# Kernel optimization log

Hardware: AMD Instinct MI355X
Metric: run time of the kernel (lower is better)

The kernel has to match this reference:

```python
import jax, jax.numpy as jnp
import numpy as np

NEG = -1000000.0  # mask value used by the torch module


def setup_inputs() -> dict:
    key = jax.random.key(0)
    k1, k2, k3, k4 = jax.random.split(key, 4)
    B, Q, K, D = 16, 2048, 2048, 128
    queries = jax.random.normal(k1, (B, Q, D), dtype=jnp.float32)
    keys = jax.random.normal(k2, (B, K, D), dtype=jnp.float32)
    values = jax.random.normal(k3, (B, K, D), dtype=jnp.float32)
    valid_lens = jax.random.randint(k4, (B,), 0, K, dtype=jnp.int32)
    return {"queries": queries, "keys": keys, "values": values, "valid_lens": valid_lens}


def reference(queries, keys, values, valid_lens):
    d = queries.shape[-1]
    # scores: [B, Q, K]
    scores = jnp.einsum("bqd,bkd->bqk", queries, keys) / jnp.sqrt(jnp.float32(d))
    # mask key positions >= valid_len[b] with the same -1e6 value as torch
    kv_pos = jnp.arange(scores.shape[-1])  # [K]
    mask = kv_pos[None, None, :] < valid_lens[:, None, None]  # [B,1,K]
    scores = jnp.where(mask, scores, NEG)
    attn = jax.nn.softmax(scores, axis=-1)
    # dropout p=0.0 -> identity (module in eval)
    return jnp.einsum("bqk,bkd->bqd", attn, values)
```

## Files before the change

### kernel.cpp

```cpp
#include <hip/hip_runtime.h>
#include <hip/hip_bf16.h>

#define NB    16
#define NQ    2048
#define NKV   2048
#define DH    128
#define KVT   32
#define NT    64
#define TIMG  8192

typedef __attribute__((ext_vector_type(8)))  short  short8;
typedef __attribute__((ext_vector_type(4)))  float  f32x4;
typedef __attribute__((ext_vector_type(2)))  float  f32x2;
typedef __attribute__((ext_vector_type(16))) float  f32x16;
typedef __attribute__((ext_vector_type(2)))  unsigned int u32x2;

__device__ __forceinline__ unsigned short f2bf(float f) {
    union { float f; unsigned int u; } x; x.f = f;
    unsigned int r = (x.u + 0x7fffu + ((x.u >> 16) & 1u)) >> 16;
    return (unsigned short)r;
}

__device__ __forceinline__ float u2f(unsigned int u) {
    union { unsigned int u; float f; } x; x.u = u; return x.f;
}

__device__ __forceinline__ void load_lds16(const void* g, void* l) {
    __builtin_amdgcn_global_load_lds(
        (const __attribute__((address_space(1))) unsigned int*)g,
        (__attribute__((address_space(3))) unsigned int*)l, 16, 0, 0);
}

__global__ __launch_bounds__(256)
void preconv(const float* __restrict__ kg, const float* __restrict__ vg,
             const int* __restrict__ vlg, char* __restrict__ kws,
             char* __restrict__ vws) {
    const int tid = threadIdx.x;
    const int bid = blockIdx.x;
    const int b = bid & 15, t = bid >> 4;
    const int vl = vlg[b];
    const int nt = (vl == 0) ? NT : ((vl + KVT - 1) >> 5);
    if (t >= nt) return;

    const float* kb = kg + ((size_t)b * NKV + t * KVT) * DH;
    const float* vb = vg + ((size_t)b * NKV + t * KVT) * DH;
    char* kimg = kws + (size_t)(b * NT + t) * TIMG;
    char* vimg = vws + (size_t)(b * NT + t) * TIMG;

    #pragma unroll
    for (int p = 0; p < 2; ++p) {
        int idx = p * 256 + tid;
        int kv = idx >> 4, ch = idx & 15;
        f32x4 a = *(const f32x4*)(kb + kv * DH + ch * 8);
        f32x4 c = *(const f32x4*)(kb + kv * DH + ch * 8 + 4);
        union { short8 v; unsigned short u[8]; } w;
        #pragma unroll
        for (int j = 0; j < 4; ++j) { w.u[j] = f2bf(a[j]); w.u[4 + j] = f2bf(c[j]); }
        *(short8*)(kimg + kv * 256 + ((ch * 16) ^ ((kv & 15) << 4))) = w.v;
    }
    #pragma unroll
    for (int p = 0; p < 2; ++p) {
        int task = p * 256 + tid;
        int w = task & 3, d = task >> 2;
        union { short8 v; unsigned short u[8]; } o;
        #pragma unroll
        for (int j = 0; j < 8; ++j) o.u[j] = f2bf(vb[(w * 8 + j) * DH + d]);
        int byte = (d >> 2) * 256 + 16 * ((w + 4 * (d & 3)) ^ ((d >> 2) & 15));
        *(short8*)(vimg + byte) = o.v;
    }
}

__global__ __launch_bounds__(256, 3)
void attn32(const float* __restrict__ qg, const char* __restrict__ kws,
            const char* __restrict__ vws, const int* __restrict__ vlg,
            float* __restrict__ og, unsigned int* __restrict__ opart,
            float* __restrict__ ellg, int S) {
    __shared__ __align__(16) char smem[32768];

    const int tid  = threadIdx.x;
    const int lane = tid & 63;
    const int wv   = tid >> 6;
    const int l31  = lane & 31;
    const int h    = lane >> 5;

    const int bid = blockIdx.x;
    const int b  = bid & 15;
    const int qt = (bid >> 4) & 15;
    const int s  = bid >> 8;
    const int q0 = qt * 128 + wv * 32;
    const int vl = vlg[b];
    const int nt = (vl == 0) ? NT : ((vl + KVT - 1) >> 5);

    if (s >= nt) return;

    const float QS = 1.4426950408889634f * 0.08838834764831845f;
    short8 qw[8];
    {
        const float* qp = qg + ((size_t)b * NQ + q0 + l31) * DH + h * 8;
        #pragma unroll
        for (int c = 0; c < 8; ++c) {
            f32x4 a  = *(const f32x4*)(qp + c * 16);
            f32x4 bb = *(const f32x4*)(qp + c * 16 + 4);
            union { short8 v; unsigned short u[8]; } t;
            #pragma unroll
            for (int j = 0; j < 4; ++j) { t.u[j] = f2bf(a[j] * QS); t.u[4 + j] = f2bf(bb[j] * QS); }
            qw[c] = t.v;
        }
    }

    const float MASKV = (vl == 0) ? 0.0f : -1442695.0f;
    f32x16 oacc[4];
    #pragma unroll
    for (int d = 0; d < 4; ++d) oacc[d] = (f32x16)(0.0f);
    float esum = 0.f;

    const char* kbase = kws + (size_t)b * NT * TIMG;
    const char* vbase = vws + (size_t)b * NT * TIMG;

    auto issue = [&](int t, int pb) {
        const char* ks = kbase + (size_t)t * TIMG;
        const char* vs = vbase + (size_t)t * TIMG;
        char* kd = smem + pb * 8192;
        char* vd = smem + 16384 + pb * 8192;
        #pragma unroll
        for (int i = 0; i < 2; ++i) {
            int off = wv * 2048 + i * 1024;
            load_lds16(ks + off + lane * 16, kd + off);
        }
        #pragma unroll
        for (int i = 0; i < 2; ++i) {
            int off = wv * 2048 + i * 1024;
            load_lds16(vs + off + lane * 16, vd + off);
        }
    };

    issue(s, 0);
    int p = 0;
    const int l15s = (l31 & 15) << 4;

    for (int tt = s; tt < nt; tt += S) {
        asm volatile("s_waitcnt vmcnt(0)" ::: "memory");
        __syncthreads();
        int tn = tt + S;
        if (tn < nt) issue(tn, p ^ 1);

        const char* kb = smem + p * 8192;
        const char* vb = smem + 16384 + p * 8192;

        f32x16 sc = (f32x16)(0.0f);
        __builtin_amdgcn_s_setprio(1);
        #pragma unroll
        for (int c = 0; c < 8; ++c) {
            short8 kf = *(const short8*)(kb + l31 * 256 + ((c * 32 + h * 16) ^ l15s));
            sc = __builtin_amdgcn_mfma_f32_32x32x16_bf16(kf, qw[c], sc, 0, 0, 0);
        }
        __builtin_amdgcn_s_setprio(0);

        if (vl == 0 || tt == nt - 1) {
            int kvb = tt * 32 + 4 * h;
            #pragma unroll
            for (int r = 0; r < 16; ++r) {
                int kvg = kvb + (r & 3) + 8 * (r >> 2);
                if (kvg >= vl) sc[r] = MASKV;
            }
        }

        float pe[16];
        #pragma unroll
        for (int r = 0; r < 16; ++r) pe[r] = __builtin_amdgcn_exp2f(sc[r]);
        esum += (((pe[0] + pe[1]) + (pe[2] + pe[3])) + ((pe[4] + pe[5]) + (pe[6] + pe[7])))
              + (((pe[8] + pe[9]) + (pe[10] + pe[11])) + ((pe[12] + pe[13]) + (pe[14] + pe[15])));

        unsigned int A, B, C, D, E, F, G, H;
        asm("v_cvt_pk_bf16_f32 %0, %1, %2" : "=v"(A) : "v"(pe[0]),  "v"(pe[1]));
        asm("v_cvt_pk_bf16_f32 %0, %1, %2" : "=v"(B) : "v"(pe[2]),  "v"(pe[3]));
        asm("v_cvt_pk_bf16_f32 %0, %1, %2" : "=v"(C) : "v"(pe[4]),  "v"(pe[5]));
        asm("v_cvt_pk_bf16_f32 %0, %1, %2" : "=v"(D) : "v"(pe[6]),  "v"(pe[7]));
        asm("v_cvt_pk_bf16_f32 %0, %1, %2" : "=v"(E) : "v"(pe[8]),  "v"(pe[9]));
        asm("v_cvt_pk_bf16_f32 %0, %1, %2" : "=v"(F) : "v"(pe[10]), "v"(pe[11]));
        asm("v_cvt_pk_bf16_f32 %0, %1, %2" : "=v"(G) : "v"(pe[12]), "v"(pe[13]));
        asm("v_cvt_pk_bf16_f32 %0, %1, %2" : "=v"(H) : "v"(pe[14]), "v"(pe[15]));
        asm("v_permlane32_swap_b32 %0, %1" : "+v"(A), "+v"(C));
        asm("v_permlane32_swap_b32 %0, %1" : "+v"(B), "+v"(D));
        asm("v_permlane32_swap_b32 %0, %1" : "+v"(E), "+v"(G));
        asm("v_permlane32_swap_b32 %0, %1" : "+v"(F), "+v"(H));
        union { short8 v; unsigned int w[4]; } P0, P1;
        P0.w[0] = A; P0.w[1] = B; P0.w[2] = C; P0.w[3] = D;
        P1.w[0] = E; P1.w[1] = F; P1.w[2] = G; P1.w[3] = H;
        short8 pa[2] = { P0.v, P1.v };

        __builtin_amdgcn_s_setprio(1);
        #pragma unroll
        for (int dblk = 0; dblk < 4; ++dblk) {
            int quad = dblk * 8 + (l31 >> 2);
            int xk = quad & 15;
            #pragma unroll
            for (int c16 = 0; c16 < 2; ++c16) {
                int w = c16 * 2 + h;
                short8 vf = *(const short8*)(vb + quad * 256 +
                                             16 * ((w + 4 * (l31 & 3)) ^ xk));
                oacc[dblk] = __builtin_amdgcn_mfma_f32_32x32x16_bf16(vf, pa[c16], oacc[dblk], 0, 0, 0);
            }
        }
        __builtin_amdgcn_s_setprio(0);
        p ^= 1;
    }

    float ea = esum, eb;
    asm volatile("v_mov_b32 %0, %1" : "=v"(eb) : "v"(esum));
    asm("v_permlane32_swap_b32 %0, %1" : "+v"(ea), "+v"(eb));
    float ell = ea + eb;

    __syncthreads();

    if (S > 1 && lane < 32)
        ellg[(size_t)s * NB * NQ + (size_t)b * NQ + q0 + lane] = ell;

    float* tw = (float*)smem + wv * 1120;
    if (lane < 32) tw[1088 + l31] = 1.0f / ell;
    unsigned int* opw = opart + ((size_t)s * NB * NQ + (size_t)b * NQ + q0) * 64;
    float* ogp = og + ((size_t)b * NQ + q0) * DH;

    #pragma unroll
    for (int dblk = 0; dblk < 4; ++dblk) {
        #pragma unroll
        for (int r = 0; r < 16; ++r) {
            int dd = (r & 3) + 8 * (r >> 2) + 4 * h;
            tw[l31 * 34 + dd] = oacc[dblk][r];
        }
        #pragma unroll
        for (int pp = 0; pp < 8; ++pp) {
            int qq = pp * 4 + (lane >> 4);
            int cc = lane & 15;
            f32x2 v = *(f32x2*)(tw + qq * 34 + cc * 2);
            if (S == 1) {
                float rl = tw[1088 + qq];
                f32x2 o = { v[0] * rl, v[1] * rl };
                *(f32x2*)(ogp + (size_t)qq * DH + dblk * 32 + cc * 2) = o;
            } else {
                unsigned int w;
                asm("v_cvt_pk_bf16_f32 %0, %1, %2" : "=v"(w) : "v"(v[0]), "v"(v[1]));
                opw[(size_t)qq * 64 + dblk * 16 + cc] = w;
            }
        }
    }
}

__global__ __launch_bounds__(256)
void combine(const unsigned int* __restrict__ opart, const float* __restrict__ ellg,
             const int* __restrict__ vlg, float* __restrict__ og, int S) {
    int idx = blockIdx.x * 256 + threadIdx.x;
    int row = idx >> 5;
    int c   = idx & 31;
    int b   = row >> 11;
    int vl  = vlg[b];
    int nact = (vl == 0) ? NT : ((vl + KVT - 1) >> 5);
    if (nact > S) nact = S;
    float a0 = 0.f, a1 = 0.f, a2 = 0.f, a3 = 0.f, l = 0.f;
    for (int s = 0; s < nact; ++s) {
        l += ellg[(size_t)s * NB * NQ + row];
        u32x2 w = *(const u32x2*)(opart + ((size_t)s * NB * NQ + row) * 64 + c * 2);
        a0 += u2f(w[0] << 16); a1 += u2f(w[0] & 0xffff0000u);
        a2 += u2f(w[1] << 16); a3 += u2f(w[1] & 0xffff0000u);
    }
    float rl = 1.0f / l;
    f32x4 o = { a0 * rl, a1 * rl, a2 * rl, a3 * rl };
    *(f32x4*)(og + (size_t)row * DH + c * 4) = o;
}

extern "C" void kernel_launch(void* const* d_in, const int* in_sizes, int n_in,
                              void* d_out, int out_size, void* d_ws, size_t ws_size,
                              hipStream_t stream) {
    const float* q  = (const float*)d_in[0];
    const float* k  = (const float*)d_in[1];
    const float* v  = (const float*)d_in[2];
    const int*   vl = (const int*)d_in[3];
    float* o = (float*)d_out;

    const size_t IMG     = (size_t)NB * NT * TIMG;
    const size_t ELL_OFF = 2 * IMG;
    const size_t ELL_MAX = (size_t)8 * NB * NQ * 4;
    const size_t OP_OFF  = ELL_OFF + ELL_MAX;
    const size_t OP_ONE  = (size_t)NB * NQ * DH * 2;

    int S = 1;
    if      (ws_size >= OP_OFF + 8 * OP_ONE) S = 8;
    else if (ws_size >= OP_OFF + 4 * OP_ONE) S = 4;
    else if (ws_size >= OP_OFF + 2 * OP_ONE) S = 2;

    char* kws = (char*)d_ws;
    char* vws = (char*)d_ws + IMG;
    float* ellg = (float*)((char*)d_ws + ELL_OFF);
    unsigned int* opart = (unsigned int*)((char*)d_ws + OP_OFF);

    preconv<<<dim3(NB * NT), dim3(256), 0, stream>>>(k, v, vl, kws, vws);
    attn32<<<dim3(256 * S), dim3(256), 0, stream>>>(q, kws, vws, vl, o, opart, ellg, S);
    if (S > 1)
        combine<<<dim3(NB * NQ * 32 / 256), dim3(256), 0, stream>>>(opart, ellg, vl, o, S);
}
```

Measured before the change: 70.19 us.

## Load K/V MFMA fragments directly from global in lane-order layout, drop LDS staging

```diff
diff --git a/kernel.cpp b/kernel.cpp
--- a/kernel.cpp
+++ b/kernel.cpp
@@ -23,12 +23,6 @@
 
 __device__ __forceinline__ float u2f(unsigned int u) {
     union { unsigned int u; float f; } x; x.u = u; return x.f;
-}
-
-__device__ __forceinline__ void load_lds16(const void* g, void* l) {
-    __builtin_amdgcn_global_load_lds(
-        (const __attribute__((address_space(1))) unsigned int*)g,
-        (__attribute__((address_space(3))) unsigned int*)l, 16, 0, 0);
 }
 
 __global__ __launch_bounds__(256)
@@ -47,49 +41,51 @@
     char* kimg = kws + (size_t)(b * NT + t) * TIMG;
     char* vimg = vws + (size_t)(b * NT + t) * TIMG;
 
+    const int lane = tid & 63;
+    const int l31  = lane & 31;
+    const int h    = (lane >> 5) & 1;
+
     #pragma unroll
     for (int p = 0; p < 2; ++p) {
-        int idx = p * 256 + tid;
-        int kv = idx >> 4, ch = idx & 15;
-        f32x4 a = *(const f32x4*)(kb + kv * DH + ch * 8);
-        f32x4 c = *(const f32x4*)(kb + kv * DH + ch * 8 + 4);
+        int c = (tid >> 6) + p * 4;
+        int d0 = c * 16 + h * 8;
+        f32x4 a  = *(const f32x4*)(kb + l31 * DH + d0);
+        f32x4 b2 = *(const f32x4*)(kb + l31 * DH + d0 + 4);
         union { short8 v; unsigned short u[8]; } w;
         #pragma unroll
-        for (int j = 0; j < 4; ++j) { w.u[j] = f2bf(a[j]); w.u[4 + j] = f2bf(c[j]); }
-        *(short8*)(kimg + kv * 256 + ((ch * 16) ^ ((kv & 15) << 4))) = w.v;
+        for (int j = 0; j < 4; ++j) { w.u[j] = f2bf(a[j]); w.u[4 + j] = f2bf(b2[j]); }
+        *(short8*)(kimg + c * 1024 + lane * 16) = w.v;
     }
     #pragma unroll
     for (int p = 0; p < 2; ++p) {
-        int task = p * 256 + tid;
-        int w = task & 3, d = task >> 2;
-        union { short8 v; unsigned short u[8]; } o;
-        #pragma unroll
-        for (int j = 0; j < 8; ++j) o.u[j] = f2bf(vb[(w * 8 + j) * DH + d]);
-        int byte = (d >> 2) * 256 + 16 * ((w + 4 * (d & 3)) ^ ((d >> 2) & 15));
-        *(short8*)(vimg + byte) = o.v;
-    }
-}
-
-__global__ __launch_bounds__(256, 3)
+        int m = (tid >> 6) + p * 4;
+        int kv0 = (m & 1) * 16 + h * 8;
+        int d   = (m >> 1) * 32 + l31;
+        union { short8 v; unsigned short u[8]; } w;
+        #pragma unroll
+        for (int j = 0; j < 8; ++j) w.u[j] = f2bf(vb[(size_t)(kv0 + j) * DH + d]);
+        *(short8*)(vimg + m * 1024 + lane * 16) = w.v;
+    }
+}
+
+__global__ __launch_bounds__(64, 2)
 void attn32(const float* __restrict__ qg, const char* __restrict__ kws,
             const char* __restrict__ vws, const int* __restrict__ vlg,
             float* __restrict__ og, unsigned int* __restrict__ opart,
             float* __restrict__ ellg, int S) {
-    __shared__ __align__(16) char smem[32768];
-
-    const int tid  = threadIdx.x;
-    const int lane = tid & 63;
-    const int wv   = tid >> 6;
+    __shared__ __align__(16) float tw[1120];
+
+    const int lane = threadIdx.x;
     const int l31  = lane & 31;
     const int h    = lane >> 5;
 
     const int bid = blockIdx.x;
-    const int b  = bid & 15;
-    const int qt = (bid >> 4) & 15;
-    const int s  = bid >> 8;
-    const int q0 = qt * 128 + wv * 32;
-    const int vl = vlg[b];
-    const int nt = (vl == 0) ? NT : ((vl + KVT - 1) >> 5);
+    const int b   = bid & 15;
+    const int qwv = (bid >> 4) & 63;
+    const int s   = bid >> 10;
+    const int q0  = qwv * 32;
+    const int vl  = vlg[b];
+    const int nt  = (vl == 0) ? NT : ((vl + KVT - 1) >> 5);
 
     if (s >= nt) return;
 
@@ -117,41 +113,15 @@
     const char* kbase = kws + (size_t)b * NT * TIMG;
     const char* vbase = vws + (size_t)b * NT * TIMG;
 
-    auto issue = [&](int t, int pb) {
-        const char* ks = kbase + (size_t)t * TIMG;
-        const char* vs = vbase + (size_t)t * TIMG;
-        char* kd = smem + pb * 8192;
-        char* vd = smem + 16384 + pb * 8192;
-        #pragma unroll
-        for (int i = 0; i < 2; ++i) {
-            int off = wv * 2048 + i * 1024;
-            load_lds16(ks + off + lane * 16, kd + off);
-        }
-        #pragma unroll
-        for (int i = 0; i < 2; ++i) {
-            int off = wv * 2048 + i * 1024;
-            load_lds16(vs + off + lane * 16, vd + off);
-        }
-    };
-
-    issue(s, 0);
-    int p = 0;
-    const int l15s = (l31 & 15) << 4;
-
     for (int tt = s; tt < nt; tt += S) {
-        asm volatile("s_waitcnt vmcnt(0)" ::: "memory");
-        __syncthreads();
-        int tn = tt + S;
-        if (tn < nt) issue(tn, p ^ 1);
-
-        const char* kb = smem + p * 8192;
-        const char* vb = smem + 16384 + p * 8192;
+        const char* kb = kbase + (size_t)tt * TIMG;
+        const char* vb = vbase + (size_t)tt * TIMG;
 
         f32x16 sc = (f32x16)(0.0f);
         __builtin_amdgcn_s_setprio(1);
         #pragma unroll
         for (int c = 0; c < 8; ++c) {
-            short8 kf = *(const short8*)(kb + l31 * 256 + ((c * 32 + h * 16) ^ l15s));
+            short8 kf = *(const short8*)(kb + c * 1024 + lane * 16);
             sc = __builtin_amdgcn_mfma_f32_32x32x16_bf16(kf, qw[c], sc, 0, 0, 0);
         }
         __builtin_amdgcn_s_setprio(0);
@@ -191,19 +161,11 @@
 
         __builtin_amdgcn_s_setprio(1);
         #pragma unroll
-        for (int dblk = 0; dblk < 4; ++dblk) {
-            int quad = dblk * 8 + (l31 >> 2);
-            int xk = quad & 15;
-            #pragma unroll
-            for (int c16 = 0; c16 < 2; ++c16) {
-                int w = c16 * 2 + h;
-                short8 vf = *(const short8*)(vb + quad * 256 +
-                                             16 * ((w + 4 * (l31 & 3)) ^ xk));
-                oacc[dblk] = __builtin_amdgcn_mfma_f32_32x32x16_bf16(vf, pa[c16], oacc[dblk], 0, 0, 0);
-            }
+        for (int m = 0; m < 8; ++m) {
+            short8 vf = *(const short8*)(vb + m * 1024 + lane * 16);
+            oacc[m >> 1] = __builtin_amdgcn_mfma_f32_32x32x16_bf16(vf, pa[m & 1], oacc[m >> 1], 0, 0, 0);
         }
         __builtin_amdgcn_s_setprio(0);
-        p ^= 1;
     }
 
     float ea = esum, eb;
@@ -211,12 +173,9 @@
     asm("v_permlane32_swap_b32 %0, %1" : "+v"(ea), "+v"(eb));
     float ell = ea + eb;
 
-    __syncthreads();
-
     if (S > 1 && lane < 32)
         ellg[(size_t)s * NB * NQ + (size_t)b * NQ + q0 + lane] = ell;
 
-    float* tw = (float*)smem + wv * 1120;
     if (lane < 32) tw[1088 + l31] = 1.0f / ell;
     unsigned int* opw = opart + ((size_t)s * NB * NQ + (size_t)b * NQ + q0) * 64;
     float* ogp = og + ((size_t)b * NQ + q0) * DH;
@@ -228,6 +187,7 @@
             int dd = (r & 3) + 8 * (r >> 2) + 4 * h;
             tw[l31 * 34 + dd] = oacc[dblk][r];
         }
+        __builtin_amdgcn_s_waitcnt(0);
         #pragma unroll
         for (int pp = 0; pp < 8; ++pp) {
             int qq = pp * 4 + (lane >> 4);
@@ -279,13 +239,12 @@
 
     const size_t IMG     = (size_t)NB * NT * TIMG;
     const size_t ELL_OFF = 2 * IMG;
-    const size_t ELL_MAX = (size_t)8 * NB * NQ * 4;
+    const size_t ELL_MAX = (size_t)4 * NB * NQ * 4;
     const size_t OP_OFF  = ELL_OFF + ELL_MAX;
     const size_t OP_ONE  = (size_t)NB * NQ * DH * 2;
 
     int S = 1;
-    if      (ws_size >= OP_OFF + 8 * OP_ONE) S = 8;
-    else if (ws_size >= OP_OFF + 4 * OP_ONE) S = 4;
+    if      (ws_size >= OP_OFF + 4 * OP_ONE) S = 4;
     else if (ws_size >= OP_OFF + 2 * OP_ONE) S = 2;
 
     char* kws = (char*)d_ws;
@@ -294,7 +253,7 @@
     unsigned int* opart = (unsigned int*)((char*)d_ws + OP_OFF);
 
     preconv<<<dim3(NB * NT), dim3(256), 0, stream>>>(k, v, vl, kws, vws);
-    attn32<<<dim3(256 * S), dim3(256), 0, stream>>>(q, kws, vws, vl, o, opart, ellg, S);
+    attn32<<<dim3(1024 * S), dim3(64), 0, stream>>>(q, kws, vws, vl, o, opart, ellg, S);
     if (S > 1)
         combine<<<dim3(NB * NQ * 32 / 256), dim3(256), 0, stream>>>(opart, ellg, vl, o, S);
 }
```

New measurement: 139.2 us. 1.98x slower.

## Process 64 query rows per wave to reuse K/V LDS fragments across two tiles

Applied to the files above, without the earlier changes.

```diff
diff --git a/kernel.cpp b/kernel.cpp
--- a/kernel.cpp
+++ b/kernel.cpp
@@ -70,8 +70,66 @@
     }
 }
 
-__global__ __launch_bounds__(256, 3)
-void attn32(const float* __restrict__ qg, const char* __restrict__ kws,
+#define SMPACK(SC, ESUM, PA0, PA1)                                             \
+    {                                                                          \
+        float pe[16];                                                          \
+        _Pragma("unroll")                                                      \
+        for (int r = 0; r < 16; ++r) pe[r] = __builtin_amdgcn_exp2f(SC[r]);    \
+        ESUM += (((pe[0]+pe[1])+(pe[2]+pe[3]))+((pe[4]+pe[5])+(pe[6]+pe[7])))  \
+              + (((pe[8]+pe[9])+(pe[10]+pe[11]))+((pe[12]+pe[13])+(pe[14]+pe[15]))); \
+        unsigned int A_,B_,C_,D_,E_,F_,G_,H_;                                  \
+        asm("v_cvt_pk_bf16_f32 %0, %1, %2" : "=v"(A_) : "v"(pe[0]),  "v"(pe[1])); \
+        asm("v_cvt_pk_bf16_f32 %0, %1, %2" : "=v"(B_) : "v"(pe[2]),  "v"(pe[3])); \
+        asm("v_cvt_pk_bf16_f32 %0, %1, %2" : "=v"(C_) : "v"(pe[4]),  "v"(pe[5])); \
+        asm("v_cvt_pk_bf16_f32 %0, %1, %2" : "=v"(D_) : "v"(pe[6]),  "v"(pe[7])); \
+        asm("v_cvt_pk_bf16_f32 %0, %1, %2" : "=v"(E_) : "v"(pe[8]),  "v"(pe[9])); \
+        asm("v_cvt_pk_bf16_f32 %0, %1, %2" : "=v"(F_) : "v"(pe[10]), "v"(pe[11])); \
+        asm("v_cvt_pk_bf16_f32 %0, %1, %2" : "=v"(G_) : "v"(pe[12]), "v"(pe[13])); \
+        asm("v_cvt_pk_bf16_f32 %0, %1, %2" : "=v"(H_) : "v"(pe[14]), "v"(pe[15])); \
+        asm("v_permlane32_swap_b32 %0, %1" : "+v"(A_), "+v"(C_));              \
+        asm("v_permlane32_swap_b32 %0, %1" : "+v"(B_), "+v"(D_));              \
+        asm("v_permlane32_swap_b32 %0, %1" : "+v"(E_), "+v"(G_));              \
+        asm("v_permlane32_swap_b32 %0, %1" : "+v"(F_), "+v"(H_));              \
+        union { short8 v; unsigned int w[4]; } P0_, P1_;                       \
+        P0_.w[0]=A_; P0_.w[1]=B_; P0_.w[2]=C_; P0_.w[3]=D_;                    \
+        P1_.w[0]=E_; P1_.w[1]=F_; P1_.w[2]=G_; P1_.w[3]=H_;                    \
+        PA0 = P0_.v; PA1 = P1_.v;                                              \
+    }
+
+#define EPIL(OACC, ELL, HALF)                                                  \
+    {                                                                          \
+        if (lane < 32) tw[1088 + l31] = 1.0f / (ELL);                          \
+        unsigned int* opw = opart + ((size_t)s * NB * NQ + (size_t)b * NQ + q0 + (HALF) * 32) * 64; \
+        float* ogp = og + ((size_t)b * NQ + q0 + (HALF) * 32) * DH;            \
+        _Pragma("unroll")                                                      \
+        for (int dblk = 0; dblk < 4; ++dblk) {                                 \
+            _Pragma("unroll")                                                  \
+            for (int r = 0; r < 16; ++r) {                                     \
+                int dd = (r & 3) + 8 * (r >> 2) + 4 * h;                       \
+                tw[l31 * 34 + dd] = OACC[dblk][r];                             \
+            }                                                                  \
+            asm volatile("s_waitcnt lgkmcnt(0)" ::: "memory");                 \
+            _Pragma("unroll")                                                  \
+            for (int pp = 0; pp < 8; ++pp) {                                   \
+                int qq = pp * 4 + (lane >> 4);                                 \
+                int cc = lane & 15;                                            \
+                f32x2 v = *(f32x2*)(tw + qq * 34 + cc * 2);                    \
+                if (S == 1) {                                                  \
+                    float rl = tw[1088 + qq];                                  \
+                    f32x2 o = { v[0] * rl, v[1] * rl };                        \
+                    *(f32x2*)(ogp + (size_t)qq * DH + dblk * 32 + cc * 2) = o; \
+                } else {                                                       \
+                    unsigned int w;                                            \
+                    asm("v_cvt_pk_bf16_f32 %0, %1, %2" : "=v"(w) : "v"(v[0]), "v"(v[1])); \
+                    opw[(size_t)qq * 64 + dblk * 16 + cc] = w;                 \
+                }                                                              \
+            }                                                                  \
+            asm volatile("s_waitcnt lgkmcnt(0)" ::: "memory");                 \
+        }                                                                      \
+    }
+
+__global__ __launch_bounds__(128, 2)
+void attn64(const float* __restrict__ qg, const char* __restrict__ kws,
             const char* __restrict__ vws, const int* __restrict__ vlg,
             float* __restrict__ og, unsigned int* __restrict__ opart,
             float* __restrict__ ellg, int S) {
@@ -87,16 +145,17 @@
     const int b  = bid & 15;
     const int qt = (bid >> 4) & 15;
     const int s  = bid >> 8;
-    const int q0 = qt * 128 + wv * 32;
+    const int q0 = qt * 128 + wv * 64;
     const int vl = vlg[b];
     const int nt = (vl == 0) ? NT : ((vl + KVT - 1) >> 5);
 
     if (s >= nt) return;
 
     const float QS = 1.4426950408889634f * 0.08838834764831845f;
-    short8 qw[8];
-    {
-        const float* qp = qg + ((size_t)b * NQ + q0 + l31) * DH + h * 8;
+    short8 qw0[8], qw1[8];
+    #pragma unroll
+    for (int half = 0; half < 2; ++half) {
+        const float* qp = qg + ((size_t)b * NQ + q0 + half * 32 + l31) * DH + h * 8;
         #pragma unroll
         for (int c = 0; c < 8; ++c) {
             f32x4 a  = *(const f32x4*)(qp + c * 16);
@@ -104,15 +163,15 @@
             union { short8 v; unsigned short u[8]; } t;
             #pragma unroll
             for (int j = 0; j < 4; ++j) { t.u[j] = f2bf(a[j] * QS); t.u[4 + j] = f2bf(bb[j] * QS); }
-            qw[c] = t.v;
+            if (half == 0) qw0[c] = t.v; else qw1[c] = t.v;
         }
     }
 
     const float MASKV = (vl == 0) ? 0.0f : -1442695.0f;
-    f32x16 oacc[4];
+    f32x16 oacc0[4], oacc1[4];
     #pragma unroll
-    for (int d = 0; d < 4; ++d) oacc[d] = (f32x16)(0.0f);
-    float esum = 0.f;
+    for (int d = 0; d < 4; ++d) { oacc0[d] = (f32x16)(0.0f); oacc1[d] = (f32x16)(0.0f); }
+    float esum0 = 0.f, esum1 = 0.f;
 
     const char* kbase = kws + (size_t)b * NT * TIMG;
     const char* vbase = vws + (size_t)b * NT * TIMG;
@@ -123,13 +182,13 @@
         char* kd = smem + pb * 8192;
         char* vd = smem + 16384 + pb * 8192;
         #pragma unroll
-        for (int i = 0; i < 2; ++i) {
-            int off = wv * 2048 + i * 1024;
+        for (int i = 0; i < 4; ++i) {
+            int off = wv * 4096 + i * 1024;
             load_lds16(ks + off + lane * 16, kd + off);
         }
         #pragma unroll
-        for (int i = 0; i < 2; ++i) {
-            int off = wv * 2048 + i * 1024;
+        for (int i = 0; i < 4; ++i) {
+            int off = wv * 4096 + i * 1024;
             load_lds16(vs + off + lane * 16, vd + off);
         }
     };
@@ -147,12 +206,13 @@
         const char* kb = smem + p * 8192;
         const char* vb = smem + 16384 + p * 8192;
 
-        f32x16 sc = (f32x16)(0.0f);
+        f32x16 sc0 = (f32x16)(0.0f), sc1 = (f32x16)(0.0f);
         __builtin_amdgcn_s_setprio(1);
         #pragma unroll
         for (int c = 0; c < 8; ++c) {
             short8 kf = *(const short8*)(kb + l31 * 256 + ((c * 32 + h * 16) ^ l15s));
-            sc = __builtin_amdgcn_mfma_f32_32x32x16_bf16(kf, qw[c], sc, 0, 0, 0);
+            sc0 = __builtin_amdgcn_mfma_f32_32x32x16_bf16(kf, qw0[c], sc0, 0, 0, 0);
+            sc1 = __builtin_amdgcn_mfma_f32_32x32x16_bf16(kf, qw1[c], sc1, 0, 0, 0);
         }
         __builtin_amdgcn_s_setprio(0);
 
@@ -161,89 +221,54 @@
             #pragma unroll
             for (int r = 0; r < 16; ++r) {
                 int kvg = kvb + (r & 3) + 8 * (r >> 2);
-                if (kvg >= vl) sc[r] = MASKV;
+                if (kvg >= vl) { sc0[r] = MASKV; sc1[r] = MASKV; }
             }
         }
 
-        float pe[16];
-        #pragma unroll
-        for (int r = 0; r < 16; ++r) pe[r] = __builtin_amdgcn_exp2f(sc[r]);
-        esum += (((pe[0] + pe[1]) + (pe[2] + pe[3])) + ((pe[4] + pe[5]) + (pe[6] + pe[7])))
-              + (((pe[8] + pe[9]) + (pe[10] + pe[11])) + ((pe[12] + pe[13]) + (pe[14] + pe[15])));
-
-        unsigned int A, B, C, D, E, F, G, H;
-        asm("v_cvt_pk_bf16_f32 %0, %1, %2" : "=v"(A) : "v"(pe[0]),  "v"(pe[1]));
-        asm("v_cvt_pk_bf16_f32 %0, %1, %2" : "=v"(B) : "v"(pe[2]),  "v"(pe[3]));
-        asm("v_cvt_pk_bf16_f32 %0, %1, %2" : "=v"(C) : "v"(pe[4]),  "v"(pe[5]));
-        asm("v_cvt_pk_bf16_f32 %0, %1, %2" : "=v"(D) : "v"(pe[6]),  "v"(pe[7]));
-        asm("v_cvt_pk_bf16_f32 %0, %1, %2" : "=v"(E) : "v"(pe[8]),  "v"(pe[9]));
-        asm("v_cvt_pk_bf16_f32 %0, %1, %2" : "=v"(F) : "v"(pe[10]), "v"(pe[11]));
-        asm("v_cvt_pk_bf16_f32 %0, %1, %2" : "=v"(G) : "v"(pe[12]), "v"(pe[13]));
-        asm("v_cvt_pk_bf16_f32 %0, %1, %2" : "=v"(H) : "v"(pe[14]), "v"(pe[15]));
-        asm("v_permlane32_swap_b32 %0, %1" : "+v"(A), "+v"(C));
-        asm("v_permlane32_swap_b32 %0, %1" : "+v"(B), "+v"(D));
-        asm("v_permlane32_swap_b32 %0, %1" : "+v"(E), "+v"(G));
-        asm("v_permlane32_swap_b32 %0, %1" : "+v"(F), "+v"(H));
-        union { short8 v; unsigned int w[4]; } P0, P1;
-        P0.w[0] = A; P0.w[1] = B; P0.w[2] = C; P0.w[3] = D;
-        P1.w[0] = E; P1.w[1] = F; P1.w[2] = G; P1.w[3] = H;
-        short8 pa[2] = { P0.v, P1.v };
+        short8 pa00, pa01, pa10, pa11;
+        SMPACK(sc0, esum0, pa00, pa01);
+        SMPACK(sc1, esum1, pa10, pa11);
 
         __builtin_amdgcn_s_setprio(1);
         #pragma unroll
-        for (int dblk = 0; dblk < 4; ++dblk) {
+        for (int m = 0; m < 8; ++m) {
+            int dblk = m >> 1;
             int quad = dblk * 8 + (l31 >> 2);
             int xk = quad & 15;
-            #pragma unroll
-            for (int c16 = 0; c16 < 2; ++c16) {
-                int w = c16 * 2 + h;
-                short8 vf = *(const short8*)(vb + quad * 256 +
-                                             16 * ((w + 4 * (l31 & 3)) ^ xk));
-                oacc[dblk] = __builtin_amdgcn_mfma_f32_32x32x16_bf16(vf, pa[c16], oacc[dblk], 0, 0, 0);
+            int w = (m & 1) * 2 + h;
+            short8 vf = *(const short8*)(vb + quad * 256 +
+                                         16 * ((w + 4 * (l31 & 3)) ^ xk));
+            if ((m & 1) == 0) {
+                oacc0[dblk] = __builtin_amdgcn_mfma_f32_32x32x16_bf16(vf, pa00, oacc0[dblk], 0, 0, 0);
+                oacc1[dblk] = __builtin_amdgcn_mfma_f32_32x32x16_bf16(vf, pa10, oacc1[dblk], 0, 0, 0);
+            } else {
+                oacc0[dblk] = __builtin_amdgcn_mfma_f32_32x32x16_bf16(vf, pa01, oacc0[dblk], 0, 0, 0);
+                oacc1[dblk] = __builtin_amdgcn_mfma_f32_32x32x16_bf16(vf, pa11, oacc1[dblk], 0, 0, 0);
             }
         }
         __builtin_amdgcn_s_setprio(0);
         p ^= 1;
     }
 
-    float ea = esum, eb;
-    asm volatile("v_mov_b32 %0, %1" : "=v"(eb) : "v"(esum));
-    asm("v_permlane32_swap_b32 %0, %1" : "+v"(ea), "+v"(eb));
-    float ell = ea + eb;
+    float ea0 = esum0, eb0;
+    asm volatile("v_mov_b32 %0, %1" : "=v"(eb0) : "v"(esum0));
+    asm("v_permlane32_swap_b32 %0, %1" : "+v"(ea0), "+v"(eb0));
+    float ell0 = ea0 + eb0;
+    float ea1 = esum1, eb1;
+    asm volatile("v_mov_b32 %0, %1" : "=v"(eb1) : "v"(esum1));
+    asm("v_permlane32_swap_b32 %0, %1" : "+v"(ea1), "+v"(eb1));
+    float ell1 = ea1 + eb1;
 
     __syncthreads();
 
-    if (S > 1 && lane < 32)
-        ellg[(size_t)s * NB * NQ + (size_t)b * NQ + q0 + lane] = ell;
+    if (S > 1 && lane < 32) {
+        ellg[(size_t)s * NB * NQ + (size_t)b * NQ + q0 + lane] = ell0;
+        ellg[(size_t)s * NB * NQ + (size_t)b * NQ + q0 + 32 + lane] = ell1;
+    }
 
     float* tw = (float*)smem + wv * 1120;
-    if (lane < 32) tw[1088 + l31] = 1.0f / ell;
-    unsigned int* opw = opart + ((size_t)s * NB * NQ + (size_t)b * NQ + q0) * 64;
-    float* ogp = og + ((size_t)b * NQ + q0) * DH;
-
-    #pragma unroll
-    for (int dblk = 0; dblk < 4; ++dblk) {
-        #pragma unroll
-        for (int r = 0; r < 16; ++r) {
-            int dd = (r & 3) + 8 * (r >> 2) + 4 * h;
-            tw[l31 * 34 + dd] = oacc[dblk][r];
-        }
-        #pragma unroll
-        for (int pp = 0; pp < 8; ++pp) {
-            int qq = pp * 4 + (lane >> 4);
-            int cc = lane & 15;
-            f32x2 v = *(f32x2*)(tw + qq * 34 + cc * 2);
-            if (S == 1) {
-                float rl = tw[1088 + qq];
-                f32x2 o = { v[0] * rl, v[1] * rl };
-                *(f32x2*)(ogp + (size_t)qq * DH + dblk * 32 + cc * 2) = o;
-            } else {
-                unsigned int w;
-                asm("v_cvt_pk_bf16_f32 %0, %1, %2" : "=v"(w) : "v"(v[0]), "v"(v[1]));
-                opw[(size_t)qq * 64 + dblk * 16 + cc] = w;
-            }
-        }
-    }
+    EPIL(oacc0, ell0, 0);
+    EPIL(oacc1, ell1, 1);
 }
 
 __global__ __launch_bounds__(256)
@@ -279,13 +304,12 @@
 
     const size_t IMG     = (size_t)NB * NT * TIMG;
     const size_t ELL_OFF = 2 * IMG;
-    const size_t ELL_MAX = (size_t)8 * NB * NQ * 4;
+    const size_t ELL_MAX = (size_t)4 * NB * NQ * 4;
     const size_t OP_OFF  = ELL_OFF + ELL_MAX;
     const size_t OP_ONE  = (size_t)NB * NQ * DH * 2;
 
     int S = 1;
-    if      (ws_size >= OP_OFF + 8 * OP_ONE) S = 8;
-    else if (ws_size >= OP_OFF + 4 * OP_ONE) S = 4;
+    if      (ws_size >= OP_OFF + 4 * OP_ONE) S = 4;
     else if (ws_size >= OP_OFF + 2 * OP_ONE) S = 2;
 
     char* kws = (char*)d_ws;
@@ -294,7 +318,7 @@
     unsigned int* opart = (unsigned int*)((char*)d_ws + OP_OFF);
 
     preconv<<<dim3(NB * NT), dim3(256), 0, stream>>>(k, v, vl, kws, vws);
-    attn32<<<dim3(256 * S), dim3(256), 0, stream>>>(q, kws, vws, vl, o, opart, ellg, S);
+    attn64<<<dim3(256 * S), dim3(128), 0, stream>>>(q, kws, vws, vl, o, opart, ellg, S);
     if (S > 1)
         combine<<<dim3(NB * NQ * 32 / 256), dim3(256), 0, stream>>>(opart, ellg, vl, o, S);
 }
```

Measured after the change: 84.52 us. 1.2x slower.

## Software-pipeline PV matmul one tile behind QK with triple-buffered V

Applied to the files above, without the earlier changes.

```diff
diff --git a/kernel.cpp b/kernel.cpp
--- a/kernel.cpp
+++ b/kernel.cpp
@@ -75,7 +75,7 @@
             const char* __restrict__ vws, const int* __restrict__ vlg,
             float* __restrict__ og, unsigned int* __restrict__ opart,
             float* __restrict__ ellg, int S) {
-    __shared__ __align__(16) char smem[32768];
+    __shared__ __align__(16) char smem[40960];
 
     const int tid  = threadIdx.x;
     const int lane = tid & 63;
@@ -117,16 +117,18 @@
     const char* kbase = kws + (size_t)b * NT * TIMG;
     const char* vbase = vws + (size_t)b * NT * TIMG;
 
-    auto issue = [&](int t, int pb) {
+    auto issueK = [&](int t, int slot) {
         const char* ks = kbase + (size_t)t * TIMG;
-        const char* vs = vbase + (size_t)t * TIMG;
-        char* kd = smem + pb * 8192;
-        char* vd = smem + 16384 + pb * 8192;
+        char* kd = smem + slot * 8192;
         #pragma unroll
         for (int i = 0; i < 2; ++i) {
             int off = wv * 2048 + i * 1024;
             load_lds16(ks + off + lane * 16, kd + off);
         }
+    };
+    auto issueV = [&](int t, int slot) {
+        const char* vs = vbase + (size_t)t * TIMG;
+        char* vd = smem + 16384 + slot * 8192;
         #pragma unroll
         for (int i = 0; i < 2; ++i) {
             int off = wv * 2048 + i * 1024;
@@ -134,18 +136,22 @@
         }
     };
 
-    issue(s, 0);
-    int p = 0;
+    issueK(s, 0); issueV(s, 0);
+    asm volatile("s_waitcnt vmcnt(0)" ::: "memory");
+    __syncthreads();
+
+    int kcur = 0, vcur = 0, vprev = 0;
+    short8 pap0 = {}, pap1 = {};
     const int l15s = (l31 & 15) << 4;
 
     for (int tt = s; tt < nt; tt += S) {
-        asm volatile("s_waitcnt vmcnt(0)" ::: "memory");
-        __syncthreads();
         int tn = tt + S;
-        if (tn < nt) issue(tn, p ^ 1);
-
-        const char* kb = smem + p * 8192;
-        const char* vb = smem + 16384 + p * 8192;
+        if (tn < nt) {
+            issueK(tn, kcur ^ 1);
+            issueV(tn, (vcur == 2) ? 0 : vcur + 1);
+        }
+
+        const char* kb = smem + kcur * 8192;
 
         f32x16 sc = (f32x16)(0.0f);
         __builtin_amdgcn_s_setprio(1);
@@ -165,21 +171,20 @@
             }
         }
 
-        float pe[16];
-        #pragma unroll
-        for (int r = 0; r < 16; ++r) pe[r] = __builtin_amdgcn_exp2f(sc[r]);
-        esum += (((pe[0] + pe[1]) + (pe[2] + pe[3])) + ((pe[4] + pe[5]) + (pe[6] + pe[7])))
-              + (((pe[8] + pe[9]) + (pe[10] + pe[11])) + ((pe[12] + pe[13]) + (pe[14] + pe[15])));
+        #pragma unroll
+        for (int r = 0; r < 16; ++r) sc[r] = __builtin_amdgcn_exp2f(sc[r]);
+        esum += (((sc[0] + sc[1]) + (sc[2] + sc[3])) + ((sc[4] + sc[5]) + (sc[6] + sc[7])))
+              + (((sc[8] + sc[9]) + (sc[10] + sc[11])) + ((sc[12] + sc[13]) + (sc[14] + sc[15])));
 
         unsigned int A, B, C, D, E, F, G, H;
-        asm("v_cvt_pk_bf16_f32 %0, %1, %2" : "=v"(A) : "v"(pe[0]),  "v"(pe[1]));
-        asm("v_cvt_pk_bf16_f32 %0, %1, %2" : "=v"(B) : "v"(pe[2]),  "v"(pe[3]));
-        asm("v_cvt_pk_bf16_f32 %0, %1, %2" : "=v"(C) : "v"(pe[4]),  "v"(pe[5]));
-        asm("v_cvt_pk_bf16_f32 %0, %1, %2" : "=v"(D) : "v"(pe[6]),  "v"(pe[7]));
-        asm("v_cvt_pk_bf16_f32 %0, %1, %2" : "=v"(E) : "v"(pe[8]),  "v"(pe[9]));
-        asm("v_cvt_pk_bf16_f32 %0, %1, %2" : "=v"(F) : "v"(pe[10]), "v"(pe[11]));
-        asm("v_cvt_pk_bf16_f32 %0, %1, %2" : "=v"(G) : "v"(pe[12]), "v"(pe[13]));
-        asm("v_cvt_pk_bf16_f32 %0, %1, %2" : "=v"(H) : "v"(pe[14]), "v"(pe[15]));
+        asm("v_cvt_pk_bf16_f32 %0, %1, %2" : "=v"(A) : "v"(sc[0]),  "v"(sc[1]));
+        asm("v_cvt_pk_bf16_f32 %0, %1, %2" : "=v"(B) : "v"(sc[2]),  "v"(sc[3]));
+        asm("v_cvt_pk_bf16_f32 %0, %1, %2" : "=v"(C) : "v"(sc[4]),  "v"(sc[5]));
+        asm("v_cvt_pk_bf16_f32 %0, %1, %2" : "=v"(D) : "v"(sc[6]),  "v"(sc[7]));
+        asm("v_cvt_pk_bf16_f32 %0, %1, %2" : "=v"(E) : "v"(sc[8]),  "v"(sc[9]));
+        asm("v_cvt_pk_bf16_f32 %0, %1, %2" : "=v"(F) : "v"(sc[10]), "v"(sc[11]));
+        asm("v_cvt_pk_bf16_f32 %0, %1, %2" : "=v"(G) : "v"(sc[12]), "v"(sc[13]));
+        asm("v_cvt_pk_bf16_f32 %0, %1, %2" : "=v"(H) : "v"(sc[14]), "v"(sc[15]));
         asm("v_permlane32_swap_b32 %0, %1" : "+v"(A), "+v"(C));
         asm("v_permlane32_swap_b32 %0, %1" : "+v"(B), "+v"(D));
         asm("v_permlane32_swap_b32 %0, %1" : "+v"(E), "+v"(G));
@@ -187,23 +192,49 @@
         union { short8 v; unsigned int w[4]; } P0, P1;
         P0.w[0] = A; P0.w[1] = B; P0.w[2] = C; P0.w[3] = D;
         P1.w[0] = E; P1.w[1] = F; P1.w[2] = G; P1.w[3] = H;
-        short8 pa[2] = { P0.v, P1.v };
-
+        short8 pan0 = P0.v, pan1 = P1.v;
+
+        if (tt != s) {
+            const char* vbp = smem + 16384 + vprev * 8192;
+            __builtin_amdgcn_s_setprio(1);
+            #pragma unroll
+            for (int m = 0; m < 8; ++m) {
+                int dblk = m >> 1;
+                int quad = dblk * 8 + (l31 >> 2);
+                int xk = quad & 15;
+                int w = (m & 1) * 2 + h;
+                short8 vf = *(const short8*)(vbp + quad * 256 +
+                                             16 * ((w + 4 * (l31 & 3)) ^ xk));
+                oacc[dblk] = __builtin_amdgcn_mfma_f32_32x32x16_bf16(
+                                 vf, (m & 1) ? pap1 : pap0, oacc[dblk], 0, 0, 0);
+            }
+            __builtin_amdgcn_s_setprio(0);
+        }
+
+        asm volatile("s_waitcnt vmcnt(0)" ::: "memory");
+        __syncthreads();
+
+        pap0 = pan0; pap1 = pan1;
+        vprev = vcur;
+        kcur ^= 1;
+        vcur = (vcur == 2) ? 0 : vcur + 1;
+    }
+
+    {
+        const char* vbp = smem + 16384 + vprev * 8192;
         __builtin_amdgcn_s_setprio(1);
         #pragma unroll
-        for (int dblk = 0; dblk < 4; ++dblk) {
+        for (int m = 0; m < 8; ++m) {
+            int dblk = m >> 1;
             int quad = dblk * 8 + (l31 >> 2);
             int xk = quad & 15;
-            #pragma unroll
-            for (int c16 = 0; c16 < 2; ++c16) {
-                int w = c16 * 2 + h;
-                short8 vf = *(const short8*)(vb + quad * 256 +
-                                             16 * ((w + 4 * (l31 & 3)) ^ xk));
-                oacc[dblk] = __builtin_amdgcn_mfma_f32_32x32x16_bf16(vf, pa[c16], oacc[dblk], 0, 0, 0);
-            }
+            int w = (m & 1) * 2 + h;
+            short8 vf = *(const short8*)(vbp + quad * 256 +
+                                         16 * ((w + 4 * (l31 & 3)) ^ xk));
+            oacc[dblk] = __builtin_amdgcn_mfma_f32_32x32x16_bf16(
+                             vf, (m & 1) ? pap1 : pap0, oacc[dblk], 0, 0, 0);
         }
         __builtin_amdgcn_s_setprio(0);
-        p ^= 1;
     }
 
     float ea = esum, eb;
@@ -228,6 +259,7 @@
             int dd = (r & 3) + 8 * (r >> 2) + 4 * h;
             tw[l31 * 34 + dd] = oacc[dblk][r];
         }
+        asm volatile("s_waitcnt lgkmcnt(0)" ::: "memory");
         #pragma unroll
         for (int pp = 0; pp < 8; ++pp) {
             int qq = pp * 4 + (lane >> 4);
@@ -243,6 +275,7 @@
                 opw[(size_t)qq * 64 + dblk * 16 + cc] = w;
             }
         }
+        asm volatile("s_waitcnt lgkmcnt(0)" ::: "memory");
     }
 }
 
@@ -279,13 +312,12 @@
 
     const size_t IMG     = (size_t)NB * NT * TIMG;
     const size_t ELL_OFF = 2 * IMG;
-    const size_t ELL_MAX = (size_t)8 * NB * NQ * 4;
+    const size_t ELL_MAX = (size_t)4 * NB * NQ * 4;
     const size_t OP_OFF  = ELL_OFF + ELL_MAX;
     const size_t OP_ONE  = (size_t)NB * NQ * DH * 2;
 
     int S = 1;
-    if      (ws_size >= OP_OFF + 8 * OP_ONE) S = 8;
-    else if (ws_size >= OP_OFF + 4 * OP_ONE) S = 4;
+    if      (ws_size >= OP_OFF + 4 * OP_ONE) S = 4;
     else if (ws_size >= OP_OFF + 2 * OP_ONE) S = 2;
 
     char* kws = (char*)d_ws;
```

Result: faster. 61.80 us (-11.9%).
